# Performance work log

Hardware: AMD Instinct MI355X
Metric: run time of the kernel (lower is better)

Reference implementation:

```python
import jax, jax.numpy as jnp
import numpy as np

# ProjectorConfig defaults
MIN_SPEECH_FRAMES = 1.0
MAX_SPEECH_EXPAND = 3.0
TAIL_HOLD_UNITS = 2
BOUNDARY_COMMIT_THRESHOLD = 0.45

B, U = 4096, 2048


def setup_inputs() -> dict:
    key = jax.random.key(0)
    ks = jax.random.split(key, 10)
    # ragged prefix mask: random visible length per row (faithful to streaming use)
    lengths = jax.random.randint(ks[0], (B,), 1, U + 1)
    unit_mask = (jnp.arange(U)[None, :] < lengths[:, None]).astype(jnp.float32)
    dur_anchor_src = jax.random.uniform(ks[1], (B, U), jnp.float32) * 20.0
    dur_logratio_unit = jax.random.normal(ks[2], (B, U), jnp.float32) * 0.3
    pause_weight_unit = jax.random.uniform(ks[3], (B, U), jnp.float32)
    boundary_latent = jax.random.uniform(ks[4], (B, U), jnp.float32)
    speech_budget_win = jax.random.uniform(ks[5], (B, 1), jnp.float32) * float(U) * 10.0
    pause_budget_win = jax.random.uniform(ks[6], (B, 1), jnp.float32) * float(U)
    open_run_mask = jax.random.bernoulli(ks[7], 0.1, (B, U)).astype(jnp.int32)
    return {
        "dur_anchor_src": dur_anchor_src,
        "unit_mask": unit_mask,
        "speech_budget_win": speech_budget_win,
        "pause_budget_win": pause_budget_win,
        "dur_logratio_unit": dur_logratio_unit,
        "pause_weight_unit": pause_weight_unit,
        "boundary_latent": boundary_latent,
        "phase_ptr": jnp.zeros((B,), jnp.float32),
        "backlog": jnp.zeros((B,), jnp.float32),
        "clock_delta": jnp.zeros((B,), jnp.float32),
        "commit_frontier": jnp.zeros((B,), jnp.int32),
        "open_run_mask": open_run_mask,
    }


def reference(dur_anchor_src, unit_mask, speech_budget_win, pause_budget_win,
              dur_logratio_unit, pause_weight_unit, boundary_latent,
              phase_ptr, backlog, clock_delta, commit_frontier, open_run_mask):
    b, u = unit_mask.shape

    # ---- _project_speech ----
    anchor = jnp.maximum(dur_anchor_src, MIN_SPEECH_FRAMES)
    base = anchor * jnp.exp(dur_logratio_unit)
    speech = jnp.maximum(jnp.minimum(base, anchor * MAX_SPEECH_EXPAND), MIN_SPEECH_FRAMES) * unit_mask
    total = jnp.maximum((speech * unit_mask).sum(axis=1, keepdims=True), 1e-6)
    speech = speech * (speech_budget_win / total) * unit_mask

    # ---- _project_pause ----
    scores = jnp.maximum(pause_weight_unit, 0.0) * (0.5 + boundary_latent) * unit_mask
    score_total = scores.sum(axis=1, keepdims=True)
    fallback = unit_mask / jnp.maximum(unit_mask.sum(axis=1, keepdims=True), 1.0)
    weights = jnp.where(score_total > 0, scores / jnp.maximum(score_total, 1e-6), fallback)
    pause = weights * pause_budget_win

    effective = (speech + pause) * unit_mask

    # ---- _compute_commit_frontier (vectorized) ----
    visible = unit_mask.sum(axis=1).astype(jnp.int32)                 # active_len [B]
    idx = jnp.arange(u, dtype=jnp.int32)[None, :]
    open_vis = (open_run_mask > 0) & (idx < visible[:, None])
    has_open = open_vis.any(axis=1)
    first_open = jnp.argmax(open_vis, axis=1).astype(jnp.int32)
    closed_prefix = jnp.where(has_open, first_open, visible)          # leading closed run
    release_cap = jnp.maximum(visible - TAIL_HOLD_UNITS, 0)
    candidate = jnp.minimum(release_cap, closed_prefix)
    prev = commit_frontier.astype(jnp.int32)
    b_idx = jnp.clip(candidate - 1, 0, u - 1)
    b_val = jnp.take_along_axis(boundary_latent, b_idx[:, None], axis=1)[:, 0]
    soft = (candidate > 0) & (candidate < visible) & (b_val < BOUNDARY_COMMIT_THRESHOLD)
    candidate = jnp.where(soft, jnp.maximum(prev, candidate - 1), candidate)
    commit = jnp.maximum(prev, candidate)

    # ---- _advance_state (prefix sums instead of python loops) ----
    zeros_col = jnp.zeros((b, 1), effective.dtype)
    cs_eff = jnp.concatenate([zeros_col, jnp.cumsum(effective, axis=1)], axis=1)
    cs_src = jnp.concatenate([zeros_col, jnp.cumsum(dur_anchor_src, axis=1)], axis=1)
    take = lambda cs, i: jnp.take_along_axis(cs, i[:, None], axis=1)[:, 0]
    exec_prefix = take(cs_eff, commit) - take(cs_eff, prev)
    src_prefix = take(cs_src, commit) - take(cs_src, prev)
    adv = commit > prev
    delta = exec_prefix - src_prefix
    next_clock = jnp.where(adv, clock_delta + delta, clock_delta)
    next_backlog = jnp.where(adv, jnp.maximum(next_clock, 0.0), backlog)
    visible_total = jnp.maximum(effective.sum(axis=1), 1.0)
    next_phase = jnp.where(adv, jnp.clip(phase_ptr + exec_prefix / visible_total, 0.0, 1.0), phase_ptr)

    return (speech, pause, effective, commit, next_phase, next_backlog, next_clock)
```

## Files before the change

### kernel.cpp

```cpp
#include <hip/hip_runtime.h>
#include <climits>


constexpr int UNITS = 2048;
constexpr int BLOCK = 256;

typedef float f32x4 __attribute__((ext_vector_type(4)));

static __device__ __forceinline__ float waveSum(float v) {
#pragma unroll
  for (int m = 1; m < 64; m <<= 1) v += __shfl_xor(v, m, 64);
  return v;
}

__global__ __launch_bounds__(BLOCK, 8) void rhythm_kernel(
    const float* __restrict__ dur_anchor,
    const float* __restrict__ unit_mask,
    const float* __restrict__ speech_budget,
    const float* __restrict__ pause_budget,
    const float* __restrict__ dur_logratio,
    const float* __restrict__ pause_weight,
    const float* __restrict__ boundary,
    const float* __restrict__ phase_ptr,
    const float* __restrict__ backlog,
    const float* __restrict__ clock_delta,
    const int*   __restrict__ commit_front,
    const int*   __restrict__ open_run,
    float* __restrict__ out,
    int B) {
  const int row = blockIdx.x;
  const int t = threadIdx.x;
  const int wv = t >> 6, ln = t & 63;
  const size_t base = (size_t)row * UNITS;

  const int prev = commit_front[row];
  const float sb = speech_budget[row];
  const float pb = pause_budget[row];

  int visible;
  {
    const int i = (ln < 32) ? ln : 0;
    const float v1 = unit_mask[base + 64 * i + 63];
    const int c1 = __popcll(__ballot((ln < 32) && (v1 > 0.5f)));
    if (c1 == 32) {
      visible = 2048;
    } else {
      const int s = 64 * c1;
      const float v2 = unit_mask[base + s + ln];
      visible = s + __popcll(__ballot(v2 > 0.5f));
    }
  }

  int min_open = INT_MAX;
  for (int cs = 0; cs < visible; cs += 256) {
    const int e = cs + 4 * ln;
    int4 o4 = make_int4(0, 0, 0, 0);
    if (e < visible) o4 = *(const int4*)(open_run + base + e);
    int lm = INT_MAX;
    if (o4.w > 0 && e + 3 < visible) lm = e + 3;
    if (o4.z > 0 && e + 2 < visible) lm = e + 2;
    if (o4.y > 0 && e + 1 < visible) lm = e + 1;
    if (o4.x > 0 && e < visible) lm = e;
    const unsigned long long bb = __ballot(lm != INT_MAX);
    if (bb) {
      min_open = __shfl(lm, (int)__ffsll(bb) - 1, 64);
      break;
    }
  }

  float sv_sr[8];
  float sv_sc[8];
  float sum_sr = 0.f, sum_sc = 0.f;

#pragma unroll
  for (int c = 0; c < 2; ++c) {
    const int e0 = c * 1024 + 4 * t;
    if (e0 < visible) {
      const float4 a4 = *(const float4*)(dur_anchor   + base + e0);
      const float4 l4 = *(const float4*)(dur_logratio + base + e0);
      const float4 p4 = *(const float4*)(pause_weight + base + e0);
      const float4 b4 = *(const float4*)(boundary     + base + e0);
      const float av[4] = {a4.x, a4.y, a4.z, a4.w};
      const float lv[4] = {l4.x, l4.y, l4.z, l4.w};
      const float pv[4] = {p4.x, p4.y, p4.z, p4.w};
      const float bv[4] = {b4.x, b4.y, b4.z, b4.w};
#pragma unroll
      for (int j = 0; j < 4; ++j) {
        const int k = c * 4 + j;
        const float m = (e0 + j < visible) ? 1.0f : 0.0f;
        const float a = fmaxf(av[j], 1.0f);
        const float sr = fmaxf(fminf(a * __expf(lv[j]), 3.0f * a), 1.0f) * m;
        const float sc = fmaxf(pv[j], 0.0f) * (0.5f + bv[j]) * m;
        sv_sr[k] = sr;
        sv_sc[k] = sc;
        sum_sr += sr;
        sum_sc += sc;
      }
    } else {
#pragma unroll
      for (int j = 0; j < 4; ++j) { sv_sr[c * 4 + j] = 0.f; sv_sc[c * 4 + j] = 0.f; }
    }
  }

  __shared__ float sf[2][4];
  const float r0 = waveSum(sum_sr);
  const float r1 = waveSum(sum_sc);
  if (ln == 0) { sf[0][wv] = r0; sf[1][wv] = r1; }
  __syncthreads();

  const float ts = sf[0][0] + sf[0][1] + sf[0][2] + sf[0][3];
  const float tc = sf[1][0] + sf[1][1] + sf[1][2] + sf[1][3];
  const float tm = (float)visible;

  const int closed = (min_open == INT_MAX) ? visible : min_open;
  const int relcap = max(visible - 2, 0);
  int cand = min(relcap, closed);
  const int bidx = min(max(cand - 1, 0), UNITS - 1);
  const float bval = boundary[base + bidx];
  if (cand > 0 && cand < visible && bval < 0.45f)
    cand = max(prev, cand - 1);
  const int commit = max(prev, cand);

  const float sscale = sb / fmaxf(ts, 1e-6f);
  const bool usefb = !(tc > 0.0f);
  const float pscale = pb / fmaxf(tc, 1e-6f);
  const float fbw = pb / fmaxf(tm, 1.0f);
  const float eff_tot = usefb ? (sscale * ts + fbw * tm) : (sscale * ts + pscale * tc);

  float* __restrict__ out_speech = out;
  float* __restrict__ out_pause  = out + (size_t)B * UNITS;
  float* __restrict__ out_eff    = out + 2 * (size_t)B * UNITS;

#pragma unroll
  for (int c = 0; c < 2; ++c) {
    const int e0 = c * 1024 + 4 * t;
    f32x4 s4, q4, e4;
#pragma unroll
    for (int j = 0; j < 4; ++j) {
      const int k = c * 4 + j;
      const float m = (e0 + j < visible) ? 1.0f : 0.0f;
      const float speech = sv_sr[k] * sscale;
      const float pause = usefb ? (m * fbw) : (sv_sc[k] * pscale);
      s4[j] = speech;
      q4[j] = pause;
      e4[j] = speech + pause;
    }
    __builtin_nontemporal_store(s4, (f32x4*)(out_speech + base + e0));
    __builtin_nontemporal_store(q4, (f32x4*)(out_pause + base + e0));
    __builtin_nontemporal_store(e4, (f32x4*)(out_eff + base + e0));
  }

  if (wv == 0) {
    float src_rng = 0.f, eff_rng = 0.f;
    if (commit > prev) {
      for (int i = prev + ln; i < commit; i += 64) {
        const float a = dur_anchor[base + i];
        const float l = dur_logratio[base + i];
        const float p = pause_weight[base + i];
        const float bo = boundary[base + i];
        src_rng += a;
        const float aa = fmaxf(a, 1.0f);
        const float sr = fmaxf(fminf(aa * __expf(l), 3.0f * aa), 1.0f);
        const float sc = fmaxf(p, 0.0f) * (0.5f + bo);
        eff_rng += sr * sscale + (usefb ? fbw : sc * pscale);
      }
    }
    const float srcp = waveSum(src_rng);
    const float execp = waveSum(eff_rng);

    if (ln == 0) {
      const float pp = phase_ptr[row];
      const float bl = backlog[row];
      const float cd = clock_delta[row];
      const bool adv = commit > prev;
      const float nclock = adv ? (cd + (execp - srcp)) : cd;
      const float nback = adv ? fmaxf(nclock, 0.0f) : bl;
      const float vt = fmaxf(eff_tot, 1.0f);
      const float nphase =
          adv ? fminf(fmaxf(pp + execp / vt, 0.0f), 1.0f) : pp;
      const size_t o = 3 * (size_t)B * UNITS;
      out[o + row] = (float)commit;
      out[o + (size_t)B + row] = nphase;
      out[o + 2 * (size_t)B + row] = nback;
      out[o + 3 * (size_t)B + row] = nclock;
    }
  }
}

extern "C" void kernel_launch(void* const* d_in, const int* in_sizes, int n_in,
                              void* d_out, int out_size, void* d_ws, size_t ws_size,
                              hipStream_t stream) {
  const int B = in_sizes[7];
  rhythm_kernel<<<dim3(B), dim3(BLOCK), 0, stream>>>(
      (const float*)d_in[0],
      (const float*)d_in[1],
      (const float*)d_in[2],
      (const float*)d_in[3],
      (const float*)d_in[4],
      (const float*)d_in[5],
      (const float*)d_in[6],
      (const float*)d_in[7],
      (const float*)d_in[8],
      (const float*)d_in[9],
      (const int*)d_in[10],
      (const int*)d_in[11],
      (float*)d_out, B);
}
```

Before: 245.2 us.

## Halve block size, hoist first-chunk loads ahead of the visible-length scan

Shrinks the per-row block from 256 to 128 threads so each thread handles four chunks of four elements, and issues the unit-mask probe, first open_run vector and first chunk of the four input arrays up front, before the dependent visible-length and open-run scans. The commit-candidate boundary load is also moved ahead of the block reduction. The aim is to overlap the serial dependency chain at the start of each row with the bulk loads and to raise memory-level parallelism per thread. In exchange it uses more registers per thread and issues the first-chunk loads without checking visibility, which is safe only because rows are always fully allocated.

```diff
diff --git a/kernel.cpp b/kernel.cpp
--- a/kernel.cpp
+++ b/kernel.cpp
@@ -3,7 +3,7 @@
 
 
 constexpr int UNITS = 2048;
-constexpr int BLOCK = 256;
+constexpr int BLOCK = 128;
 
 typedef float f32x4 __attribute__((ext_vector_type(4)));
 
@@ -37,10 +37,16 @@
   const float sb = speech_budget[row];
   const float pb = pause_budget[row];
 
+  const float v1 = unit_mask[base + 64 * ((ln < 32) ? ln : 0) + 63];
+  const int4 o4_0 = *(const int4*)(open_run + base + 4 * ln);
+  const int e0c0 = 4 * t;
+  const float4 a0 = *(const float4*)(dur_anchor   + base + e0c0);
+  const float4 l0 = *(const float4*)(dur_logratio + base + e0c0);
+  const float4 p0 = *(const float4*)(pause_weight + base + e0c0);
+  const float4 b0 = *(const float4*)(boundary     + base + e0c0);
+
   int visible;
   {
-    const int i = (ln < 32) ? ln : 0;
-    const float v1 = unit_mask[base + 64 * i + 63];
     const int c1 = __popcll(__ballot((ln < 32) && (v1 > 0.5f)));
     if (c1 == 32) {
       visible = 2048;
@@ -52,29 +58,66 @@
   }
 
   int min_open = INT_MAX;
-  for (int cs = 0; cs < visible; cs += 256) {
-    const int e = cs + 4 * ln;
-    int4 o4 = make_int4(0, 0, 0, 0);
-    if (e < visible) o4 = *(const int4*)(open_run + base + e);
+  {
+    const int e = 4 * ln;
     int lm = INT_MAX;
-    if (o4.w > 0 && e + 3 < visible) lm = e + 3;
-    if (o4.z > 0 && e + 2 < visible) lm = e + 2;
-    if (o4.y > 0 && e + 1 < visible) lm = e + 1;
-    if (o4.x > 0 && e < visible) lm = e;
+    if (o4_0.w > 0 && e + 3 < visible) lm = e + 3;
+    if (o4_0.z > 0 && e + 2 < visible) lm = e + 2;
+    if (o4_0.y > 0 && e + 1 < visible) lm = e + 1;
+    if (o4_0.x > 0 && e < visible)     lm = e;
     const unsigned long long bb = __ballot(lm != INT_MAX);
     if (bb) {
       min_open = __shfl(lm, (int)__ffsll(bb) - 1, 64);
-      break;
-    }
-  }
-
-  float sv_sr[8];
-  float sv_sc[8];
+    } else {
+      for (int cs = 256; cs < visible; cs += 256) {
+        const int e2 = cs + 4 * ln;
+        int4 o4 = make_int4(0, 0, 0, 0);
+        if (e2 < visible) o4 = *(const int4*)(open_run + base + e2);
+        int lm2 = INT_MAX;
+        if (o4.w > 0 && e2 + 3 < visible) lm2 = e2 + 3;
+        if (o4.z > 0 && e2 + 2 < visible) lm2 = e2 + 2;
+        if (o4.y > 0 && e2 + 1 < visible) lm2 = e2 + 1;
+        if (o4.x > 0 && e2 < visible)     lm2 = e2;
+        const unsigned long long bb2 = __ballot(lm2 != INT_MAX);
+        if (bb2) {
+          min_open = __shfl(lm2, (int)__ffsll(bb2) - 1, 64);
+          break;
+        }
+      }
+    }
+  }
+
+  const int closed = (min_open == INT_MAX) ? visible : min_open;
+  const int relcap = max(visible - 2, 0);
+  const int cand0 = min(relcap, closed);
+  const int bidx = min(max(cand0 - 1, 0), UNITS - 1);
+  const float bval = boundary[base + bidx];
+
+  float sv_sr[16];
+  float sv_sc[16];
   float sum_sr = 0.f, sum_sc = 0.f;
 
-#pragma unroll
-  for (int c = 0; c < 2; ++c) {
-    const int e0 = c * 1024 + 4 * t;
+  {
+    const float av[4] = {a0.x, a0.y, a0.z, a0.w};
+    const float lv[4] = {l0.x, l0.y, l0.z, l0.w};
+    const float pv[4] = {p0.x, p0.y, p0.z, p0.w};
+    const float bv[4] = {b0.x, b0.y, b0.z, b0.w};
+#pragma unroll
+    for (int j = 0; j < 4; ++j) {
+      const float m = (e0c0 + j < visible) ? 1.0f : 0.0f;
+      const float a = fmaxf(av[j], 1.0f);
+      const float sr = fmaxf(fminf(a * __expf(lv[j]), 3.0f * a), 1.0f) * m;
+      const float sc = fmaxf(pv[j], 0.0f) * (0.5f + bv[j]) * m;
+      sv_sr[j] = sr;
+      sv_sc[j] = sc;
+      sum_sr += sr;
+      sum_sc += sc;
+    }
+  }
+
+#pragma unroll
+  for (int c = 1; c < 4; ++c) {
+    const int e0 = c * 512 + 4 * t;
     if (e0 < visible) {
       const float4 a4 = *(const float4*)(dur_anchor   + base + e0);
       const float4 l4 = *(const float4*)(dur_logratio + base + e0);
@@ -102,23 +145,19 @@
     }
   }
 
-  __shared__ float sf[2][4];
+  __shared__ float sf[2][2];
   const float r0 = waveSum(sum_sr);
   const float r1 = waveSum(sum_sc);
   if (ln == 0) { sf[0][wv] = r0; sf[1][wv] = r1; }
   __syncthreads();
 
-  const float ts = sf[0][0] + sf[0][1] + sf[0][2] + sf[0][3];
-  const float tc = sf[1][0] + sf[1][1] + sf[1][2] + sf[1][3];
+  const float ts = sf[0][0] + sf[0][1];
+  const float tc = sf[1][0] + sf[1][1];
   const float tm = (float)visible;
 
-  const int closed = (min_open == INT_MAX) ? visible : min_open;
-  const int relcap = max(visible - 2, 0);
-  int cand = min(relcap, closed);
-  const int bidx = min(max(cand - 1, 0), UNITS - 1);
-  const float bval = boundary[base + bidx];
-  if (cand > 0 && cand < visible && bval < 0.45f)
-    cand = max(prev, cand - 1);
+  int cand = cand0;
+  if (cand0 > 0 && cand0 < visible && bval < 0.45f)
+    cand = max(prev, cand0 - 1);
   const int commit = max(prev, cand);
 
   const float sscale = sb / fmaxf(ts, 1e-6f);
@@ -132,8 +171,8 @@
   float* __restrict__ out_eff    = out + 2 * (size_t)B * UNITS;
 
 #pragma unroll
-  for (int c = 0; c < 2; ++c) {
-    const int e0 = c * 1024 + 4 * t;
+  for (int c = 0; c < 4; ++c) {
+    const int e0 = c * 512 + 4 * t;
     f32x4 s4, q4, e4;
 #pragma unroll
     for (int j = 0; j < 4; ++j) {
```

Measured after the change: 254.3 us. 3.7% more time.
